# Kernel tuning notes

Hardware: AMD Instinct MI355X
Metric: run time of the kernel (lower is better)

The kernel has to match this reference:

```python
import jax, jax.numpy as jnp
import numpy as np
import math

CHANNELS = 1024
NUM_HEADS = 16
HEAD_DIM = CHANNELS // NUM_HEADS  # 64
ROPE_DIM = int(HEAD_DIM * 0.5)    # 32
BASE_FREQ = 10000.0


def apply_rope(x):
    """x: [b, h, t, d]; rotate first ROPE_DIM features, pass the rest through."""
    t = x.shape[2]
    half = ROPE_DIM // 2
    theta = 1.0 / (BASE_FREQ ** (jnp.arange(0, ROPE_DIM, 2, dtype=jnp.float32) / ROPE_DIM))  # [half]
    ang = jnp.arange(t, dtype=jnp.float32)[:, None] * theta[None, :]  # [t, half]
    ang = jnp.concatenate([ang, ang], axis=-1)  # [t, ROPE_DIM]
    cos = jnp.cos(ang)[None, None, :, :]
    sin = jnp.sin(ang)[None, None, :, :]
    x_rope, x_pass = x[..., :ROPE_DIM], x[..., ROPE_DIM:]
    neg_half = jnp.concatenate([-x_rope[..., half:], x_rope[..., :half]], axis=-1)
    x_rope = x_rope * cos + neg_half * sin
    return jnp.concatenate([x_rope, x_pass], axis=-1)


def proximal_bias(length):
    pos = jnp.arange(length, dtype=jnp.float32)
    diff = pos[None, :] - pos[:, None]
    return -jnp.log1p(jnp.abs(diff))[None, None, :, :]  # [1,1,t,t]


def conv1x1(x, w, b):
    """x: [b, c_in, t], w: [c_out, c_in], b: [c_out] -> [b, c_out, t]"""
    return jnp.einsum('oc,bct->bot', w, x) + b[None, :, None]


def setup_inputs() -> dict:
    key = jax.random.key(0)
    ks = jax.random.split(key, 10)
    B, C, T = 8, CHANNELS, 1024
    scale = 1.0 / math.sqrt(C)
    return {
        "x": jax.random.normal(ks[0], (B, C, T), dtype=jnp.float32),
        "context": jax.random.normal(ks[1], (B, C, T), dtype=jnp.float32),
        "attention_mask": jnp.ones((B, 1, 1, T), dtype=jnp.int32),
        "Wq": jax.random.normal(ks[2], (C, C), dtype=jnp.float32) * scale,
        "bq": jnp.zeros((C,), dtype=jnp.float32),
        "Wk": jax.random.normal(ks[3], (C, C), dtype=jnp.float32) * scale,
        "bk": jnp.zeros((C,), dtype=jnp.float32),
        "Wv": jax.random.normal(ks[4], (C, C), dtype=jnp.float32) * scale,
        "bv": jnp.zeros((C,), dtype=jnp.float32),
        "Wo": jax.random.normal(ks[5], (C, C), dtype=jnp.float32) * scale,
        "bo": jnp.zeros((C,), dtype=jnp.float32),
    }


def reference(x, context, attention_mask, Wq, bq, Wk, bk, Wv, bv, Wo, bo):
    B, C, T = x.shape
    H, D = NUM_HEADS, HEAD_DIM
    q = conv1x1(x, Wq, bq)
    k = conv1x1(context, Wk, bk)
    v = conv1x1(context, Wv, bv)
    # b (h d) t -> b h t d
    def split_heads(z):
        return z.reshape(B, H, D, -1).transpose(0, 1, 3, 2)
    q, k, v = split_heads(q), split_heads(k), split_heads(v)
    q = apply_rope(q)
    k = apply_rope(k)
    scores = jnp.einsum('bhqd,bhkd->bhqk', q, k) / math.sqrt(D)
    scores = scores + proximal_bias(T)  # proximal_bias=True, self-attention
    scores = jnp.where(attention_mask == 0, jnp.float32(-10000.0), scores)
    probs = jax.nn.softmax(scores, axis=-1)  # dropout_rate=0.0 -> identity
    out = jnp.einsum('bhqk,bhkd->bhqd', probs, v)
    # b h q d -> b (h d) q
    out = out.transpose(0, 1, 3, 2).reshape(B, C, T)
    return conv1x1(out, Wo, bo)
```

## Files before the change

kernel.cpp:

```cpp
#include <hip/hip_runtime.h>
#include <hip/hip_bf16.h>
#include <math.h>

#define BB 8
#define CC 1024
#define TT 1024
#define HH 16
#define DD 64

typedef __attribute__((ext_vector_type(8))) short short8;
typedef __attribute__((ext_vector_type(4))) short short4_;
typedef __attribute__((ext_vector_type(4))) float f32x4;
typedef __attribute__((ext_vector_type(4))) int   i32x4;
typedef __attribute__((ext_vector_type(2))) unsigned long long u64x2;

#define QSCALE 0.18033688f

__device__ __forceinline__ unsigned short f2bf(float f) {
    unsigned u = __builtin_bit_cast(unsigned, f);
    u += 0x7fffu + ((u >> 16) & 1u);
    return (unsigned short)(u >> 16);
}

__device__ __forceinline__ f32x4 mfma16(short8 a, short8 b, f32x4 c) {
    return __builtin_amdgcn_mfma_f32_16x16x32_bf16(a, b, c, 0, 0, 0);
}

__device__ __forceinline__ void async16(const void* g, void* l) {
    __builtin_amdgcn_global_load_lds(
        (const __attribute__((address_space(1))) unsigned int*)g,
        (__attribute__((address_space(3))) unsigned int*)l, 16, 0, 0);
}

__device__ __forceinline__ unsigned cvtpk(float lo, float hi) {
    unsigned r;
    asm("v_cvt_pk_bf16_f32 %0, %1, %2" : "=v"(r) : "v"(lo), "v"(hi));
    return r;
}

__global__ __launch_bounds__(256) void cast_w_kernel(
    const float* __restrict__ Wq, const float* __restrict__ Wk,
    const float* __restrict__ Wv, const float* __restrict__ Wo,
    unsigned short* __restrict__ dst)
{
    const int z = blockIdx.y;
    const float* W = (z == 0) ? Wq : (z == 1) ? Wk : (z == 2) ? Wv : Wo;
    unsigned short* d = dst + (size_t)z * CC * CC;
    int idx = blockIdx.x * 256 + threadIdx.x;
    float4 f = ((const float4*)W)[idx];
    short4_ s;
    s[0] = (short)f2bf(f.x); s[1] = (short)f2bf(f.y);
    s[2] = (short)f2bf(f.z); s[3] = (short)f2bf(f.w);
    ((short4_*)d)[idx] = s;
}

__global__ __launch_bounds__(256) void tcast2_kernel(
    const float* __restrict__ x, const float* __restrict__ ctx,
    unsigned short* __restrict__ xT, unsigned short* __restrict__ cTo)
{
    __shared__ float sT[64][65];
    const int tid = threadIdx.x;
    const int z = blockIdx.z;
    const float* in = (z < BB) ? x : ctx;
    unsigned short* out = (z < BB) ? xT : cTo;
    const int b = (z < BB) ? z : z - BB;
    const int tB = blockIdx.x * 64, cT = blockIdx.y * 64;

    const float* ib = in + ((size_t)b * CC + cT) * TT + tB;
    const int r = tid >> 2;
    #pragma unroll
    for (int j = 0; j < 4; j++) {
        int t4 = (tid & 3) * 4 + j * 16;
        float4 f = *(const float4*)(ib + (size_t)r * TT + t4);
        sT[r][t4 + 0] = f.x; sT[r][t4 + 1] = f.y;
        sT[r][t4 + 2] = f.z; sT[r][t4 + 3] = f.w;
    }
    __syncthreads();
    const int t_l = tid >> 2, cch = (tid & 3) * 16;
    short8 o0, o1;
    #pragma unroll
    for (int i = 0; i < 8; i++) {
        o0[i] = (short)f2bf(sT[cch + i][t_l]);
        o1[i] = (short)f2bf(sT[cch + 8 + i][t_l]);
    }
    unsigned short* dp = out + ((size_t)b * TT + tB + t_l) * CC + cT + cch;
    *(short8*)dp = o0;
    *(short8*)(dp + 8) = o1;
}

__global__ __launch_bounds__(256) void tcast_kernel(
    const float* __restrict__ in, unsigned short* __restrict__ out)
{
    __shared__ float sT[64][65];
    const int tid = threadIdx.x;
    const int tB = blockIdx.x * 64, cT = blockIdx.y * 64, b = blockIdx.z;

    const float* ib = in + ((size_t)b * CC + cT) * TT + tB;
    const int r = tid >> 2;
    #pragma unroll
    for (int j = 0; j < 4; j++) {
        int t4 = (tid & 3) * 4 + j * 16;
        float4 f = *(const float4*)(ib + (size_t)r * TT + t4);
        sT[r][t4 + 0] = f.x; sT[r][t4 + 1] = f.y;
        sT[r][t4 + 2] = f.z; sT[r][t4 + 3] = f.w;
    }
    __syncthreads();
    const int t_l = tid >> 2, cch = (tid & 3) * 16;
    short8 o0, o1;
    #pragma unroll
    for (int i = 0; i < 8; i++) {
        o0[i] = (short)f2bf(sT[cch + i][t_l]);
        o1[i] = (short)f2bf(sT[cch + 8 + i][t_l]);
    }
    unsigned short* dp = out + ((size_t)b * TT + tB + t_l) * CC + cT + cch;
    *(short8*)dp = o0;
    *(short8*)(dp + 8) = o1;
}

__global__ __launch_bounds__(256) void qkv_gll_kernel(
    const unsigned short* __restrict__ xT, const unsigned short* __restrict__ cT,
    const unsigned short* __restrict__ Wq2, const unsigned short* __restrict__ Wk2,
    const unsigned short* __restrict__ Wv2,
    const float* __restrict__ bq, const float* __restrict__ bk,
    const float* __restrict__ bv,
    unsigned short* __restrict__ qo, unsigned short* __restrict__ ko,
    unsigned short* __restrict__ vo,
    int mode)
{
    __shared__ __align__(16) short smem[4 * 64 * 72];

    const int tid = threadIdx.x, lane = tid & 63, wave = tid >> 6;
    const int wm = wave >> 1, wn = wave & 1;
    const int l15 = lane & 15, lq = lane >> 4;

    const int zz = blockIdx.x, tTile = blockIdx.y, oTile = blockIdx.z;
    int w, b;
    if (mode == 0)      { w = zz % 3;        b = zz / 3;  }
    else if (mode == 1) { w = 0;             b = zz;      }
    else                { w = 1 + (zz & 1);  b = zz >> 1; }
    const unsigned short* inT = (w == 0) ? xT : cT;
    const int oBase = oTile * 128, tBase = tTile * 128;

    const unsigned short* WA = (w == 0) ? Wq2 : (w == 1) ? Wk2 : Wv2;
    const float* bias        = (w == 0) ? bq  : (w == 1) ? bk  : bv;

    const int srow = lane >> 2;
    const int sch  = (lane ^ (lane >> 2) ^ (lane >> 4)) & 3;
    const unsigned short* gA0 = WA + (size_t)(oBase + wave * 32 + srow) * CC + sch * 8;
    const unsigned short* gA1 = gA0 + (size_t)16 * CC;
    const unsigned short* gB0 = inT + ((size_t)b * TT + tBase + wave * 32 + srow) * CC + sch * 8;
    const unsigned short* gB1 = gB0 + (size_t)16 * CC;

    short* A0b = smem;            short* B0b = smem + 4096;
    short* A1b = smem + 8192;     short* B1b = smem + 12288;
    const int oA0 = (wave * 2 + 0) * 512;
    const int oA1 = (wave * 2 + 1) * 512;

    const int csw = ((lq ^ (l15 & 3) ^ (l15 >> 2)) & 3) * 8;

    f32x4 acc[4][4];
    #pragma unroll
    for (int mt = 0; mt < 4; mt++)
        #pragma unroll
        for (int nt = 0; nt < 4; nt++) acc[mt][nt] = (f32x4){0.f, 0.f, 0.f, 0.f};

    auto stage = [&](int c0, short* dA, short* dB) {
        async16(gA0 + c0, dA + oA0);
        async16(gA1 + c0, dA + oA1);
        async16(gB0 + c0, dB + oA0);
        async16(gB1 + c0, dB + oA1);
    };
    auto compute = [&](const short* bA, const short* bB) {
        short8 af[4], bf[4];
        #pragma unroll
        for (int mt = 0; mt < 4; mt++)
            af[mt] = *(const short8*)(bA + (wm * 64 + mt * 16 + l15) * 32 + csw);
        #pragma unroll
        for (int nt = 0; nt < 4; nt++)
            bf[nt] = *(const short8*)(bB + (wn * 64 + nt * 16 + l15) * 32 + csw);
        #pragma unroll
        for (int mt = 0; mt < 4; mt++)
            #pragma unroll
            for (int nt = 0; nt < 4; nt++)
                acc[mt][nt] = mfma16(af[mt], bf[nt], acc[mt][nt]);
    };

    stage(0, A0b, B0b);

    #pragma unroll 1
    for (int tt = 0; tt < 16; tt++) {
        const int c = tt * 64;
        asm volatile("s_waitcnt vmcnt(0)" ::: "memory");
        __builtin_amdgcn_s_barrier();
        __builtin_amdgcn_sched_barrier(0);
        stage(c + 32, A1b, B1b);
        compute(A0b, B0b);
        asm volatile("s_waitcnt lgkmcnt(0)" ::: "memory");

        asm volatile("s_waitcnt vmcnt(0)" ::: "memory");
        __builtin_amdgcn_s_barrier();
        __builtin_amdgcn_sched_barrier(0);
        if (tt < 15) stage(c + 64, A0b, B0b);
        compute(A1b, B1b);
        asm volatile("s_waitcnt lgkmcnt(0)" ::: "memory");
    }
    __syncthreads();

    #pragma unroll
    for (int mt = 0; mt < 4; mt++)
        #pragma unroll
        for (int r = 0; r < 4; r++) {
            float bi = bias[oBase + wm * 64 + mt * 16 + lq * 4 + r];
            #pragma unroll
            for (int nt = 0; nt < 4; nt++) {
                acc[mt][nt][r] += bi;
                if (w == 0) acc[mt][nt][r] *= QSCALE;
            }
        }

    const int h = oTile * 2 + wm;
    short* sT = smem + wave * (64 * 72);

    if (w < 2) {
        #pragma unroll
        for (int r = 0; r < 4; r++) {
            float dr = (float)(lq * 4 + r);
            float theta = exp2f(dr * -0.8304820237f);
            float sa, ca, ss, cs;
            sincosf((float)(tBase + wn * 64 + l15) * theta, &sa, &ca);
            sincosf(16.0f * theta, &ss, &cs);
            #pragma unroll
            for (int nt = 0; nt < 4; nt++) {
                float x0 = acc[0][nt][r], x1 = acc[1][nt][r];
                acc[0][nt][r] = x0 * ca - x1 * sa;
                acc[1][nt][r] = x1 * ca + x0 * sa;
                float c2 = ca * cs - sa * ss;
                sa = sa * cs + ca * ss;
                ca = c2;
            }
        }
        #pragma unroll
        for (int nt = 0; nt < 4; nt++)
            #pragma unroll
            for (int mt = 0; mt < 4; mt++) {
                short4_ v4;
                #pragma unroll
                for (int r = 0; r < 4; r++) v4[r] = (short)f2bf(acc[mt][nt][r]);
                *(short4_*)(sT + (nt * 16 + l15) * 72 + mt * 16 + lq * 4) = v4;
            }
    } else {
        #pragma unroll
        for (int mt = 0; mt < 4; mt++)
            #pragma unroll
            for (int r = 0; r < 4; r++)
                #pragma unroll
                for (int nt = 0; nt < 4; nt++)
                    sT[(mt * 16 + lq * 4 + r) * 72 + nt * 16 + l15] =
                        (short)f2bf(acc[mt][nt][r]);
    }
    __asm__ volatile("s_waitcnt lgkmcnt(0)" ::: "memory");

    unsigned short* dstBase;
    if (w == 0)
        dstBase = qo + ((size_t)(b * HH + h) * TT + tBase + wn * 64 + lane) * DD;
    else if (w == 1)
        dstBase = ko + ((size_t)(b * HH + h) * TT + tBase + wn * 64 + lane) * DD;
    else
        dstBase = vo + ((size_t)(b * HH + h) * DD + lane) * TT + tBase + wn * 64;
    #pragma unroll
    for (int j = 0; j < 8; j++)
        *(short8*)(dstBase + j * 8) = *(short8*)(sT + lane * 72 + j * 8);
}

__global__ __launch_bounds__(256) void oproj_gll_kernel(
    const unsigned short* __restrict__ att, const unsigned short* __restrict__ Wo2,
    const float* __restrict__ bo, float* __restrict__ out)
{
    __shared__ __align__(16) short smem[16384];

    const int tid = threadIdx.x, lane = tid & 63, wave = tid >> 6;
    const int wm = wave >> 1, wn = wave & 1;
    const int l15 = lane & 15, lq = lane >> 4;
    const int b = blockIdx.x, tTile = blockIdx.y, oTile = blockIdx.z;
    const int oBase = oTile * 128, tBase = tTile * 128;

    const int srow = lane >> 2;
    const int sch  = (lane ^ (lane >> 2) ^ (lane >> 4)) & 3;
    const unsigned short* gA0 = Wo2 + (size_t)(oBase + wave * 32 + srow) * CC + sch * 8;
    const unsigned short* gA1 = gA0 + (size_t)16 * CC;
    const unsigned short* attB = att + (size_t)b * HH * TT * DD;
    const int t0 = tBase + wave * 32 + srow;
    const int csch = sch * 8;

    short* A0b = smem;            short* B0b = smem + 4096;
    short* A1b = smem + 8192;     short* B1b = smem + 12288;
    const int oA0 = (wave * 2 + 0) * 512;
    const int oA1 = (wave * 2 + 1) * 512;

    const int csw = ((lq ^ (l15 & 3) ^ (l15 >> 2)) & 3) * 8;

    f32x4 acc[4][4];
    #pragma unroll
    for (int mt = 0; mt < 4; mt++)
        #pragma unroll
        for (int nt = 0; nt < 4; nt++) acc[mt][nt] = (f32x4){0.f, 0.f, 0.f, 0.f};

    auto stage = [&](int c0, short* dA, short* dB) {
        int c = c0 + csch;
        const unsigned short* g0 =
            attB + ((size_t)(c >> 6) * TT + t0) * DD + (c & 63);
        async16(gA0 + c0, dA + oA0);
        async16(gA1 + c0, dA + oA1);
        async16(g0, dB + oA0);
        async16(g0 + 16 * DD, dB + oA1);
    };
    auto compute = [&](const short* bA, const short* bB) {
        short8 af[4], bf[4];
        #pragma unroll
        for (int mt = 0; mt < 4; mt++)
            af[mt] = *(const short8*)(bA + (wm * 64 + mt * 16 + l15) * 32 + csw);
        #pragma unroll
        for (int nt = 0; nt < 4; nt++)
            bf[nt] = *(const short8*)(bB + (wn * 64 + nt * 16 + l15) * 32 + csw);
        #pragma unroll
        for (int mt = 0; mt < 4; mt++)
            #pragma unroll
            for (int nt = 0; nt < 4; nt++)
                acc[mt][nt] = mfma16(af[mt], bf[nt], acc[mt][nt]);
    };

    stage(0, A0b, B0b);

    #pragma unroll 1
    for (int tt = 0; tt < 16; tt++) {
        const int c = tt * 64;
        asm volatile("s_waitcnt vmcnt(0)" ::: "memory");
        __builtin_amdgcn_s_barrier();
        __builtin_amdgcn_sched_barrier(0);
        stage(c + 32, A1b, B1b);
        compute(A0b, B0b);
        asm volatile("s_waitcnt lgkmcnt(0)" ::: "memory");

        asm volatile("s_waitcnt vmcnt(0)" ::: "memory");
        __builtin_amdgcn_s_barrier();
        __builtin_amdgcn_sched_barrier(0);
        if (tt < 15) stage(c + 64, A0b, B0b);
        compute(A1b, B1b);
        asm volatile("s_waitcnt lgkmcnt(0)" ::: "memory");
    }

    #pragma unroll
    for (int mt = 0; mt < 4; mt++)
        #pragma unroll
        for (int r = 0; r < 4; r++) {
            int o = oBase + wm * 64 + mt * 16 + lq * 4 + r;
            float bi = bo[o];
            float* dst = out + ((size_t)b * CC + o) * TT + tBase + wn * 64;
            #pragma unroll
            for (int nt = 0; nt < 4; nt++)
                dst[nt * 16 + l15] = acc[mt][nt][r] + bi;
        }
}

__global__ __launch_bounds__(256) void attn_mfma_kernel(
    const unsigned short* __restrict__ q, const unsigned short* __restrict__ k,
    const unsigned short* __restrict__ v, const int* __restrict__ mask,
    unsigned short* __restrict__ att)
{
    __shared__ __align__(16) short sQw[64 * 72];
    __shared__ __align__(16) short sK[64 * 72];
    __shared__ __align__(16) short sV[64 * 72];
    __shared__ int sOK[4];

    const int tid = threadIdx.x, lane = tid & 63, wq = tid >> 6;
    const int l15 = lane & 15, lq = lane >> 4;
    const int bh = blockIdx.x, qTile = blockIdx.y, b = bh >> 4;

    const int sr = tid >> 2, sc = (tid & 3) * 16;
    const int* maskB = mask + b * TT;

    {
        i32x4 m4 = *(const i32x4*)(maskB + tid * 4);
        int ok = (m4[0] != 0) & (m4[1] != 0) & (m4[2] != 0) & (m4[3] != 0);
        unsigned long long bal = __ballot(ok);
        if (lane == 0) sOK[wq] = (bal == ~0ull);
    }

    {
        const unsigned short* gq = q + ((size_t)bh * TT + qTile * 64 + sr) * DD + sc;
        *(short8*)(sQw + sr * 72 + sc)     = *(const short8*)gq;
        *(short8*)(sQw + sr * 72 + sc + 8) = *(const short8*)(gq + 8);
    }
    __syncthreads();

    const short8 bq0 = *(short8*)(sQw + (wq * 16 + l15) * 72 + lq * 8);
    const short8 bq1 = *(short8*)(sQw + (wq * 16 + l15) * 72 + 32 + lq * 8);
    const bool allOK = sOK[0] && sOK[1] && sOK[2] && sOK[3];
    __syncthreads();

    float* wtab = (float*)sQw;
    #pragma unroll
    for (int j = 0; j < 8; j++) {
        int d = tid + 256 * j;
        int ad = d - 1023; ad = ad < 0 ? -ad : ad;
        wtab[d] = __builtin_amdgcn_rcpf(1.0f + (float)ad);
    }

    short8 vones;
    #pragma unroll
    for (int e = 0; e < 8; e++) vones[e] = (short)0x3F80;

    f32x4 accO[4];
    #pragma unroll
    for (int nt = 0; nt < 4; nt++) accO[nt] = (f32x4){0.f, 0.f, 0.f, 0.f};
    f32x4 accD = (f32x4){0.f, 0.f, 0.f, 0.f};

    const int qpos = qTile * 64 + wq * 16 + l15;
    const unsigned short* kB = k + (size_t)bh * TT * DD;
    const unsigned short* vB = v + (size_t)bh * DD * TT;

    const int xo = ((tid & 3) >> 1) * 8 + (tid & 1) * 4;
    short* vwp = sV + sr * 72 + xo;

    const unsigned short* gk = kB + (size_t)sr * DD + sc;
    const unsigned short* gv = vB + (size_t)sr * TT + sc;
    short8 kr0 = *(const short8*)gk;
    short8 kr1 = *(const short8*)(gk + 8);
    short8 vr0 = *(const short8*)gv;
    short8 vr1 = *(const short8*)(gv + 8);

    for (int kt = 0; kt < 16; kt++) {
        __syncthreads();
        *(short8*)(sK + sr * 72 + sc)     = kr0;
        *(short8*)(sK + sr * 72 + sc + 8) = kr1;
        {
            u64x2 vv0 = __builtin_bit_cast(u64x2, vr0);
            u64x2 vv1 = __builtin_bit_cast(u64x2, vr1);
            *(unsigned long long*)(vwp)      = vv0[0];
            *(unsigned long long*)(vwp + 16) = vv0[1];
            *(unsigned long long*)(vwp + 32) = vv1[0];
            *(unsigned long long*)(vwp + 48) = vv1[1];
        }
        __syncthreads();

        if (kt < 15) {
            gk += 64 * DD;
            gv += 64;
            kr0 = *(const short8*)gk;
            kr1 = *(const short8*)(gk + 8);
            vr0 = *(const short8*)gv;
            vr1 = *(const short8*)(gv + 8);
        }

        f32x4 s4[4];
        #pragma unroll
        for (int nt = 0; nt < 4; nt++) {
            short8 ka0 = *(short8*)(sK + (nt * 16 + l15) * 72 + lq * 8);
            short8 ka1 = *(short8*)(sK + (nt * 16 + l15) * 72 + 32 + lq * 8);
            f32x4 z = (f32x4){0.f, 0.f, 0.f, 0.f};
            z = mfma16(ka0, bq0, z);
            z = mfma16(ka1, bq1, z);
            s4[nt] = z;
        }

        const float* wrow = wtab + (kt * 64 + lq * 4 + 1023 - qpos);
        unsigned pk8[4][2];
        if (allOK) {
            #pragma unroll
            for (int nt = 0; nt < 4; nt++) {
                #pragma unroll
                for (int h2 = 0; h2 < 2; h2++) {
                    float p0 = __builtin_amdgcn_exp2f(s4[nt][2 * h2])
                               * wrow[nt * 16 + 2 * h2];
                    float p1 = __builtin_amdgcn_exp2f(s4[nt][2 * h2 + 1])
                               * wrow[nt * 16 + 2 * h2 + 1];
                    pk8[nt][h2] = cvtpk(p0, p1);
                }
            }
        } else {
            #pragma unroll
            for (int nt = 0; nt < 4; nt++) {
                i32x4 mk = *(const i32x4*)(maskB + kt * 64 + nt * 16 + lq * 4);
                #pragma unroll
                for (int h2 = 0; h2 < 2; h2++) {
                    float p0 = __builtin_amdgcn_exp2f(s4[nt][2 * h2])
                               * wrow[nt * 16 + 2 * h2];
                    float p1 = __builtin_amdgcn_exp2f(s4[nt][2 * h2 + 1])
                               * wrow[nt * 16 + 2 * h2 + 1];
                    p0 = mk[2 * h2]     ? p0 : 0.f;
                    p1 = mk[2 * h2 + 1] ? p1 : 0.f;
                    pk8[nt][h2] = cvtpk(p0, p1);
                }
            }
        }

        i32x4 c0 = {(int)pk8[0][0], (int)pk8[0][1], (int)pk8[1][0], (int)pk8[1][1]};
        i32x4 c1 = {(int)pk8[2][0], (int)pk8[2][1], (int)pk8[3][0], (int)pk8[3][1]};
        short8 ap0 = __builtin_bit_cast(short8, c0);
        short8 ap1 = __builtin_bit_cast(short8, c1);

        accD = mfma16(ap0, vones, accD);
        accD = mfma16(ap1, vones, accD);

        #pragma unroll
        for (int nt = 0; nt < 4; nt++) {
            const short* vrow = sV + (nt * 16 + l15) * 72 + lq * 16;
            short8 b0 = *(short8*)(vrow);
            short8 b1 = *(short8*)(vrow + 8);
            accO[nt] = mfma16(ap0, b0, accO[nt]);
            accO[nt] = mfma16(ap1, b1, accO[nt]);
        }
    }

    unsigned short* aB = att + ((size_t)bh * TT + qTile * 64 + wq * 16 + lq * 4) * DD;
    #pragma unroll
    for (int r = 0; r < 4; r++) {
        float inv = 1.0f / accD[r];
        #pragma unroll
        for (int nt = 0; nt < 4; nt++)
            aB[(size_t)r * DD + nt * 16 + l15] = f2bf(accO[nt][r] * inv);
    }
}

__global__ __launch_bounds__(256) void qkv_mfma_kernel(
    const float* __restrict__ x, const float* __restrict__ ctx,
    const float* __restrict__ Wq, const float* __restrict__ bq,
    const float* __restrict__ Wk, const float* __restrict__ bk,
    const float* __restrict__ Wv, const float* __restrict__ bv,
    unsigned short* __restrict__ qo, unsigned short* __restrict__ ko,
    unsigned short* __restrict__ vo)
{
    __shared__ __align__(16) short smem[4 * 64 * 72];
    short* sA = smem;
    short* sB = smem + 128 * 40;

    const int tid  = threadIdx.x;
    const int lane = tid & 63;
    const int wave = tid >> 6;
    const int wm = wave >> 1, wn = wave & 1;
    const int l15 = lane & 15, lq = lane >> 4;

    const int tTile = blockIdx.x, oTile = blockIdx.y;
    const int b = blockIdx.z / 3, w = blockIdx.z % 3;
    const int oBase = oTile * 128, tBase = tTile * 128;

    const float* In   = (w == 0) ? x  : ctx;
    const float* W    = (w == 0) ? Wq : (w == 1) ? Wk : Wv;
    const float* bias = (w == 0) ? bq : (w == 1) ? bk : bv;
    const float* InB  = In + (size_t)b * CC * TT;

    const int ao = tid >> 1, ak = (tid & 1) * 16;
    const int bt = tid & 127, bk_ = (tid >> 7) * 16;
    const float* gA = W + (size_t)(oBase + ao) * CC + ak;
    const float* gB = InB + (size_t)bk_ * TT + tBase + bt;

    f32x4 acc[4][4];
    #pragma unroll
    for (int mt = 0; mt < 4; mt++)
        #pragma unroll
        for (int nt = 0; nt < 4; nt++) acc[mt][nt] = (f32x4){0.f, 0.f, 0.f, 0.f};

    for (int c0 = 0; c0 < CC; c0 += 32) {
        float fa[16], fb[16];
        #pragma unroll
        for (int i = 0; i < 4; i++) {
            float4 t4 = *(const float4*)(gA + c0 + 4 * i);
            fa[4*i+0] = t4.x; fa[4*i+1] = t4.y; fa[4*i+2] = t4.z; fa[4*i+3] = t4.w;
        }
        #pragma unroll
        for (int j = 0; j < 16; j++)
            fb[j] = gB[(size_t)(c0 + j) * TT];

        __syncthreads();
        short8 pa0, pa1, pb0, pb1;
        #pragma unroll
        for (int e = 0; e < 8; e++) {
            pa0[e] = (short)f2bf(fa[e]);   pa1[e] = (short)f2bf(fa[8 + e]);
            pb0[e] = (short)f2bf(fb[e]);   pb1[e] = (short)f2bf(fb[8 + e]);
        }
        *(short8*)(sA + ao * 40 + ak)     = pa0;
        *(short8*)(sA + ao * 40 + ak + 8) = pa1;
        *(short8*)(sB + bt * 40 + bk_)     = pb0;
        *(short8*)(sB + bt * 40 + bk_ + 8) = pb1;
        __syncthreads();

        short8 af[4], bf[4];
        #pragma unroll
        for (int mt = 0; mt < 4; mt++)
            af[mt] = *(short8*)(sA + (wm * 64 + mt * 16 + l15) * 40 + lq * 8);
        #pragma unroll
        for (int nt = 0; nt < 4; nt++)
            bf[nt] = *(short8*)(sB + (wn * 64 + nt * 16 + l15) * 40 + lq * 8);
        #pragma unroll
        for (int mt = 0; mt < 4; mt++)
            #pragma unroll
            for (int nt = 0; nt < 4; nt++)
                acc[mt][nt] = mfma16(af[mt], bf[nt], acc[mt][nt]);
    }

    #pragma unroll
    for (int mt = 0; mt < 4; mt++)
        #pragma unroll
        for (int r = 0; r < 4; r++) {
            float bi = bias[oBase + wm * 64 + mt * 16 + lq * 4 + r];
            #pragma unroll
            for (int nt = 0; nt < 4; nt++) {
                acc[mt][nt][r] += bi;
                if (w == 0) acc[mt][nt][r] *= QSCALE;
            }
        }

    const int h = oTile * 2 + wm;
    __syncthreads();
    short* sT = smem + wave * (64 * 72);

    if (w < 2) {
        #pragma unroll
        for (int r = 0; r < 4; r++) {
            float theta = powf(10000.0f, -(float)(lq * 4 + r) * (1.0f / 16.0f));
            #pragma unroll
            for (int nt = 0; nt < 4; nt++) {
                float tpos = (float)(tBase + wn * 64 + nt * 16 + l15);
                float sa, ca;
                sincosf(tpos * theta, &sa, &ca);
                float x0 = acc[0][nt][r], x1 = acc[1][nt][r];
                acc[0][nt][r] = x0 * ca - x1 * sa;
                acc[1][nt][r] = x1 * ca + x0 * sa;
            }
        }
        #pragma unroll
        for (int nt = 0; nt < 4; nt++)
            #pragma unroll
            for (int mt = 0; mt < 4; mt++) {
                short4_ v4;
                #pragma unroll
                for (int r = 0; r < 4; r++) v4[r] = (short)f2bf(acc[mt][nt][r]);
                *(short4_*)(sT + (nt * 16 + l15) * 72 + mt * 16 + lq * 4) = v4;
            }
    } else {
        #pragma unroll
        for (int mt = 0; mt < 4; mt++)
            #pragma unroll
            for (int r = 0; r < 4; r++)
                #pragma unroll
                for (int nt = 0; nt < 4; nt++)
                    sT[(mt * 16 + lq * 4 + r) * 72 + nt * 16 + l15] =
                        (short)f2bf(acc[mt][nt][r]);
    }
    __asm__ volatile("s_waitcnt lgkmcnt(0)" ::: "memory");

    unsigned short* dstBase;
    if (w == 0)
        dstBase = qo + ((size_t)(b * HH + h) * TT + tBase + wn * 64 + lane) * DD;
    else if (w == 1)
        dstBase = ko + ((size_t)(b * HH + h) * TT + tBase + wn * 64 + lane) * DD;
    else
        dstBase = vo + ((size_t)(b * HH + h) * DD + lane) * TT + tBase + wn * 64;
    #pragma unroll
    for (int j = 0; j < 8; j++)
        *(short8*)(dstBase + j * 8) = *(short8*)(sT + lane * 72 + j * 8);
}

__global__ __launch_bounds__(256) void oproj_mfma_kernel(
    const unsigned short* __restrict__ att, const float* __restrict__ Wo,
    const float* __restrict__ bo, float* __restrict__ out)
{
    __shared__ __align__(16) short smem[2 * 128 * 40];
    short* sA = smem;
    short* sB = smem + 128 * 40;

    const int tid = threadIdx.x, lane = tid & 63, wave = tid >> 6;
    const int wm = wave >> 1, wn = wave & 1;
    const int l15 = lane & 15, lq = lane >> 4;
    const int tTile = blockIdx.x, oTile = blockIdx.y, b = blockIdx.z;
    const int oBase = oTile * 128, tBase = tTile * 128;

    const int ao = tid >> 1, ak = (tid & 1) * 16;
    const int bt = tid & 127, bk_ = (tid >> 7) * 16;
    const float* gA = Wo + (size_t)(oBase + ao) * CC + ak;

    f32x4 acc[4][4];
    #pragma unroll
    for (int mt = 0; mt < 4; mt++)
        #pragma unroll
        for (int nt = 0; nt < 4; nt++) acc[mt][nt] = (f32x4){0.f, 0.f, 0.f, 0.f};

    for (int c0 = 0; c0 < CC; c0 += 32) {
        float fa[16];
        #pragma unroll
        for (int i = 0; i < 4; i++) {
            float4 t4 = *(const float4*)(gA + c0 + 4 * i);
            fa[4*i+0] = t4.x; fa[4*i+1] = t4.y; fa[4*i+2] = t4.z; fa[4*i+3] = t4.w;
        }
        int c = c0 + bk_;
        const unsigned short* gB =
            att + (((size_t)b * HH + (c >> 6)) * TT + tBase + bt) * DD + (c & 63);
        short8 pb0 = *(const short8*)gB;
        short8 pb1 = *(const short8*)(gB + 8);

        __syncthreads();
        short8 pa0, pa1;
        #pragma unroll
        for (int e = 0; e < 8; e++) {
            pa0[e] = (short)f2bf(fa[e]); pa1[e] = (short)f2bf(fa[8 + e]);
        }
        *(short8*)(sA + ao * 40 + ak)      = pa0;
        *(short8*)(sA + ao * 40 + ak + 8)  = pa1;
        *(short8*)(sB + bt * 40 + bk_)     = pb0;
        *(short8*)(sB + bt * 40 + bk_ + 8) = pb1;
        __syncthreads();

        short8 af[4], bf[4];
        #pragma unroll
        for (int mt = 0; mt < 4; mt++)
            af[mt] = *(short8*)(sA + (wm * 64 + mt * 16 + l15) * 40 + lq * 8);
        #pragma unroll
        for (int nt = 0; nt < 4; nt++)
            bf[nt] = *(short8*)(sB + (wn * 64 + nt * 16 + l15) * 40 + lq * 8);
        #pragma unroll
        for (int mt = 0; mt < 4; mt++)
            #pragma unroll
            for (int nt = 0; nt < 4; nt++)
                acc[mt][nt] = mfma16(af[mt], bf[nt], acc[mt][nt]);
    }

    #pragma unroll
    for (int mt = 0; mt < 4; mt++)
        #pragma unroll
        for (int r = 0; r < 4; r++) {
            int o = oBase + wm * 64 + mt * 16 + lq * 4 + r;
            float bi = bo[o];
            float* dst = out + ((size_t)b * CC + o) * TT + tBase + wn * 64;
            #pragma unroll
            for (int nt = 0; nt < 4; nt++)
                dst[nt * 16 + l15] = acc[mt][nt][r] + bi;
        }
}

extern "C" void kernel_launch(void* const* d_in, const int* in_sizes, int n_in,
                              void* d_out, int out_size, void* d_ws, size_t ws_size,
                              hipStream_t stream)
{
    const float* x   = (const float*)d_in[0];
    const float* ctx = (const float*)d_in[1];
    const int* mask  = (const int*)d_in[2];
    const float* Wq  = (const float*)d_in[3];
    const float* bq  = (const float*)d_in[4];
    const float* Wk  = (const float*)d_in[5];
    const float* bk  = (const float*)d_in[6];
    const float* Wv  = (const float*)d_in[7];
    const float* bv  = (const float*)d_in[8];
    const float* Wo  = (const float*)d_in[9];
    const float* bo  = (const float*)d_in[10];
    float* out = (float*)d_out;

    const size_t nq = (size_t)BB * HH * TT * DD;
    const size_t nw = (size_t)CC * CC;

    if (ws_size >= (5 * nq + 4 * nw) * sizeof(unsigned short)) {
        unsigned short* q   = (unsigned short*)d_ws;
        unsigned short* k   = q + nq;
        unsigned short* v   = k + nq;
        unsigned short* xT  = v + nq;
        unsigned short* cT  = xT + nq;
        unsigned short* Wb  = cT + nq;
        unsigned short* Wqb = Wb;
        unsigned short* Wkb = Wb + nw;
        unsigned short* Wvb = Wb + 2 * nw;
        unsigned short* Wob = Wb + 3 * nw;

        cast_w_kernel<<<dim3(1024, 4), 256, 0, stream>>>(Wq, Wk, Wv, Wo, Wb);
        tcast2_kernel<<<dim3(16, 16, BB * 2), 256, 0, stream>>>(x, ctx, xT, cT);
        qkv_gll_kernel<<<dim3(BB * 3, 8, 8), 256, 0, stream>>>(
            xT, cT, Wqb, Wkb, Wvb, bq, bk, bv, q, k, v, 0);
        attn_mfma_kernel<<<dim3(BB * HH, TT / 64), 256, 0, stream>>>(
            q, k, v, mask, xT);
        oproj_gll_kernel<<<dim3(BB, 8, 8), 256, 0, stream>>>(xT, Wob, bo, out);
    } else if (ws_size >= (4 * nq + 4 * nw) * sizeof(unsigned short)) {
        unsigned short* q   = (unsigned short*)d_ws;
        unsigned short* k   = q + nq;
        unsigned short* v   = k + nq;
        unsigned short* buf = v + nq;
        unsigned short* Wb  = buf + nq;
        unsigned short* Wqb = Wb;
        unsigned short* Wkb = Wb + nw;
        unsigned short* Wvb = Wb + 2 * nw;
        unsigned short* Wob = Wb + 3 * nw;

        cast_w_kernel<<<dim3(1024, 4), 256, 0, stream>>>(Wq, Wk, Wv, Wo, Wb);
        tcast_kernel<<<dim3(16, 16, BB), 256, 0, stream>>>(x, buf);
        qkv_gll_kernel<<<dim3(BB, 8, 8), 256, 0, stream>>>(
            buf, buf, Wqb, Wkb, Wvb, bq, bk, bv, q, k, v, 1);
        tcast_kernel<<<dim3(16, 16, BB), 256, 0, stream>>>(ctx, buf);
        qkv_gll_kernel<<<dim3(BB * 2, 8, 8), 256, 0, stream>>>(
            buf, buf, Wqb, Wkb, Wvb, bq, bk, bv, q, k, v, 2);
        attn_mfma_kernel<<<dim3(BB * HH, TT / 64), 256, 0, stream>>>(
            q, k, v, mask, buf);
        oproj_gll_kernel<<<dim3(BB, 8, 8), 256, 0, stream>>>(buf, Wob, bo, out);
    } else {
        unsigned short* q   = (unsigned short*)d_ws;
        unsigned short* k   = q + nq;
        unsigned short* v   = k + nq;
        unsigned short* att = v + nq;
        qkv_mfma_kernel<<<dim3(8, 8, BB * 3), 256, 0, stream>>>(
            x, ctx, Wq, bq, Wk, bk, Wv, bv, q, k, v);
        attn_mfma_kernel<<<dim3(BB * HH, TT / 64), 256, 0, stream>>>(
            q, k, v, mask, att);
        oproj_mfma_kernel<<<dim3(8, 8, BB), 256, 0, stream>>>(att, Wo, bo, out);
    }
}
```

Measured before the change: 303.3 us.

## Triple-buffer QKV GEMM loads with vmcnt-based waits and reorder grid dims

Replaces the double-buffered K-loop in the QKV projection with a three-stage ring of LDS buffers. Each step prefetches two tiles ahead and waits with partial vmcnt counts instead of draining all loads, so global-memory latency can overlap more MFMA work. The launch grid is also reordered so tile indices run fastest and batch/weight select is on z, which changes block scheduling order and L2 reuse. LDS use rises (3*8192 shorts) and the epilogue staging buffer now reuses a differently sized smem array, which could hurt occupancy or correctness if the epilogue needs more space.

```diff
diff --git a/kernel.cpp b/kernel.cpp
--- a/kernel.cpp
+++ b/kernel.cpp
@@ -127,13 +127,14 @@
     unsigned short* __restrict__ vo,
     int mode)
 {
-    __shared__ __align__(16) short smem[4 * 64 * 72];
+    __shared__ __align__(16) short smem[3 * 8192];
 
     const int tid = threadIdx.x, lane = tid & 63, wave = tid >> 6;
     const int wm = wave >> 1, wn = wave & 1;
     const int l15 = lane & 15, lq = lane >> 4;
 
-    const int zz = blockIdx.x, tTile = blockIdx.y, oTile = blockIdx.z;
+    const int tTile = blockIdx.x, oTile = blockIdx.y;
+    const int zz = blockIdx.z;
     int w, b;
     if (mode == 0)      { w = zz % 3;        b = zz / 3;  }
     else if (mode == 1) { w = 0;             b = zz;      }
@@ -151,8 +152,9 @@
     const unsigned short* gB0 = inT + ((size_t)b * TT + tBase + wave * 32 + srow) * CC + sch * 8;
     const unsigned short* gB1 = gB0 + (size_t)16 * CC;
 
-    short* A0b = smem;            short* B0b = smem + 4096;
-    short* A1b = smem + 8192;     short* B1b = smem + 12288;
+    short* cA = smem;             short* cB = smem + 4096;
+    short* nA = smem + 8192;      short* nB = smem + 12288;
+    short* pA = smem + 16384;     short* pB = smem + 20480;
     const int oA0 = (wave * 2 + 0) * 512;
     const int oA1 = (wave * 2 + 1) * 512;
 
@@ -164,47 +166,46 @@
         #pragma unroll
         for (int nt = 0; nt < 4; nt++) acc[mt][nt] = (f32x4){0.f, 0.f, 0.f, 0.f};
 
-    auto stage = [&](int c0, short* dA, short* dB) {
-        async16(gA0 + c0, dA + oA0);
-        async16(gA1 + c0, dA + oA1);
-        async16(gB0 + c0, dB + oA0);
-        async16(gB1 + c0, dB + oA1);
-    };
-    auto compute = [&](const short* bA, const short* bB) {
+    async16(gA0, cA + oA0);       async16(gA1, cA + oA1);
+    async16(gB0, cB + oA0);       async16(gB1, cB + oA1);
+    async16(gA0 + 32, nA + oA0);  async16(gA1 + 32, nA + oA1);
+    async16(gB0 + 32, nB + oA0);  async16(gB1 + 32, nB + oA1);
+
+    for (int t = 0; t < 32; t++) {
+        if (t < 30) {
+            int c2 = (t + 2) * 32;
+            async16(gA0 + c2, pA + oA0);
+            async16(gA1 + c2, pA + oA1);
+            async16(gB0 + c2, pB + oA0);
+            async16(gB1 + c2, pB + oA1);
+        }
+        __builtin_amdgcn_sched_barrier(0);
+        if (t < 30)       asm volatile("s_waitcnt vmcnt(8)" ::: "memory");
+        else if (t == 30) asm volatile("s_waitcnt vmcnt(4)" ::: "memory");
+        else              asm volatile("s_waitcnt vmcnt(0)" ::: "memory");
+        __builtin_amdgcn_s_barrier();
+        __builtin_amdgcn_sched_barrier(0);
+
         short8 af[4], bf[4];
         #pragma unroll
         for (int mt = 0; mt < 4; mt++)
-            af[mt] = *(const short8*)(bA + (wm * 64 + mt * 16 + l15) * 32 + csw);
+            af[mt] = *(short8*)(cA + (wm * 64 + mt * 16 + l15) * 32 + csw);
         #pragma unroll
         for (int nt = 0; nt < 4; nt++)
-            bf[nt] = *(const short8*)(bB + (wn * 64 + nt * 16 + l15) * 32 + csw);
+            bf[nt] = *(short8*)(cB + (wn * 64 + nt * 16 + l15) * 32 + csw);
         #pragma unroll
         for (int mt = 0; mt < 4; mt++)
             #pragma unroll
             for (int nt = 0; nt < 4; nt++)
                 acc[mt][nt] = mfma16(af[mt], bf[nt], acc[mt][nt]);
-    };
-
-    stage(0, A0b, B0b);
-
-    #pragma unroll 1
-    for (int tt = 0; tt < 16; tt++) {
-        const int c = tt * 64;
-        asm volatile("s_waitcnt vmcnt(0)" ::: "memory");
+
+        __builtin_amdgcn_sched_barrier(0);
+        asm volatile("s_waitcnt lgkmcnt(0)" ::: "memory");
         __builtin_amdgcn_s_barrier();
-        __builtin_amdgcn_sched_barrier(0);
-        stage(c + 32, A1b, B1b);
-        compute(A0b, B0b);
-        asm volatile("s_waitcnt lgkmcnt(0)" ::: "memory");
-
-        asm volatile("s_waitcnt vmcnt(0)" ::: "memory");
-        __builtin_amdgcn_s_barrier();
-        __builtin_amdgcn_sched_barrier(0);
-        if (tt < 15) stage(c + 64, A0b, B0b);
-        compute(A1b, B1b);
-        asm volatile("s_waitcnt lgkmcnt(0)" ::: "memory");
-    }
-    __syncthreads();
+
+        short* tA = cA; cA = nA; nA = pA; pA = tA;
+        short* tB = cB; cB = nB; nB = pB; pB = tB;
+    }
 
     #pragma unroll
     for (int mt = 0; mt < 4; mt++)
@@ -771,7 +772,7 @@
 
         cast_w_kernel<<<dim3(1024, 4), 256, 0, stream>>>(Wq, Wk, Wv, Wo, Wb);
         tcast2_kernel<<<dim3(16, 16, BB * 2), 256, 0, stream>>>(x, ctx, xT, cT);
-        qkv_gll_kernel<<<dim3(BB * 3, 8, 8), 256, 0, stream>>>(
+        qkv_gll_kernel<<<dim3(8, 8, BB * 3), 256, 0, stream>>>(
             xT, cT, Wqb, Wkb, Wvb, bq, bk, bv, q, k, v, 0);
         attn_mfma_kernel<<<dim3(BB * HH, TT / 64), 256, 0, stream>>>(
             q, k, v, mask, xT);
@@ -789,10 +790,10 @@
 
         cast_w_kernel<<<dim3(1024, 4), 256, 0, stream>>>(Wq, Wk, Wv, Wo, Wb);
         tcast_kernel<<<dim3(16, 16, BB), 256, 0, stream>>>(x, buf);
-        qkv_gll_kernel<<<dim3(BB, 8, 8), 256, 0, stream>>>(
+        qkv_gll_kernel<<<dim3(8, 8, BB), 256, 0, stream>>>(
             buf, buf, Wqb, Wkb, Wvb, bq, bk, bv, q, k, v, 1);
         tcast_kernel<<<dim3(16, 16, BB), 256, 0, stream>>>(ctx, buf);
-        qkv_gll_kernel<<<dim3(BB * 2, 8, 8), 256, 0, stream>>>(
+        qkv_gll_kernel<<<dim3(8, 8, BB * 2), 256, 0, stream>>>(
             buf, buf, Wqb, Wkb, Wvb, bq, bk, bv, q, k, v, 2);
         attn_mfma_kernel<<<dim3(BB * HH, TT / 64), 256, 0, stream>>>(
             q, k, v, mask, buf);
```

New measurement: 295.2 us. -2.7%, faster.

## Enlarge projection GEMM tiles to 256x128 with 512-thread blocks

Applied to the files above, without the earlier changes.

The QKV and output projection kernels move from 256-thread blocks with 128x128 output tiles to 512-thread blocks with 256x128 tiles. The input (B-side) tile is shared by 8 waves instead of 4, so each activation row is loaded half as often. The grid is reordered so tiles along t vary fastest, which may change L2 reuse of the weights. The QKV epilogue now writes through shared memory in two passes because the transpose scratch only fits 4 waves at a time, adding barriers. Larger blocks also mean fewer blocks in the grid and more LDS per block, which can lower occupancy.

```diff
diff --git a/kernel.cpp b/kernel.cpp
--- a/kernel.cpp
+++ b/kernel.cpp
@@ -117,7 +117,7 @@
     *(short8*)(dp + 8) = o1;
 }
 
-__global__ __launch_bounds__(256) void qkv_gll_kernel(
+__global__ __launch_bounds__(512) void qkv_gll_kernel(
     const unsigned short* __restrict__ xT, const unsigned short* __restrict__ cT,
     const unsigned short* __restrict__ Wq2, const unsigned short* __restrict__ Wk2,
     const unsigned short* __restrict__ Wv2,
@@ -127,19 +127,20 @@
     unsigned short* __restrict__ vo,
     int mode)
 {
-    __shared__ __align__(16) short smem[4 * 64 * 72];
+    __shared__ __align__(16) short smem[24576];
 
     const int tid = threadIdx.x, lane = tid & 63, wave = tid >> 6;
     const int wm = wave >> 1, wn = wave & 1;
     const int l15 = lane & 15, lq = lane >> 4;
 
-    const int zz = blockIdx.x, tTile = blockIdx.y, oTile = blockIdx.z;
+    const int tTile = blockIdx.x, oTile = blockIdx.y;
+    const int zz = blockIdx.z;
     int w, b;
     if (mode == 0)      { w = zz % 3;        b = zz / 3;  }
     else if (mode == 1) { w = 0;             b = zz;      }
     else                { w = 1 + (zz & 1);  b = zz >> 1; }
     const unsigned short* inT = (w == 0) ? xT : cT;
-    const int oBase = oTile * 128, tBase = tTile * 128;
+    const int oBase = oTile * 256, tBase = tTile * 128;
 
     const unsigned short* WA = (w == 0) ? Wq2 : (w == 1) ? Wk2 : Wv2;
     const float* bias        = (w == 0) ? bq  : (w == 1) ? bk  : bv;
@@ -148,13 +149,10 @@
     const int sch  = (lane ^ (lane >> 2) ^ (lane >> 4)) & 3;
     const unsigned short* gA0 = WA + (size_t)(oBase + wave * 32 + srow) * CC + sch * 8;
     const unsigned short* gA1 = gA0 + (size_t)16 * CC;
-    const unsigned short* gB0 = inT + ((size_t)b * TT + tBase + wave * 32 + srow) * CC + sch * 8;
-    const unsigned short* gB1 = gB0 + (size_t)16 * CC;
-
-    short* A0b = smem;            short* B0b = smem + 4096;
-    short* A1b = smem + 8192;     short* B1b = smem + 12288;
-    const int oA0 = (wave * 2 + 0) * 512;
-    const int oA1 = (wave * 2 + 1) * 512;
+    const unsigned short* gB0 = inT + ((size_t)b * TT + tBase + wave * 16 + srow) * CC + sch * 8;
+
+    short* b0A = smem;            short* b0B = smem + 8192;
+    short* b1A = smem + 12288;    short* b1B = smem + 20480;
 
     const int csw = ((lq ^ (l15 & 3) ^ (l15 >> 2)) & 3) * 8;
 
@@ -165,10 +163,9 @@
         for (int nt = 0; nt < 4; nt++) acc[mt][nt] = (f32x4){0.f, 0.f, 0.f, 0.f};
 
     auto stage = [&](int c0, short* dA, short* dB) {
-        async16(gA0 + c0, dA + oA0);
-        async16(gA1 + c0, dA + oA1);
-        async16(gB0 + c0, dB + oA0);
-        async16(gB1 + c0, dB + oA1);
+        async16(gA0 + c0, dA + (wave * 2 + 0) * 512);
+        async16(gA1 + c0, dA + (wave * 2 + 1) * 512);
+        async16(gB0 + c0, dB + wave * 512);
     };
     auto compute = [&](const short* bA, const short* bB) {
         short8 af[4], bf[4];
@@ -185,7 +182,7 @@
                 acc[mt][nt] = mfma16(af[mt], bf[nt], acc[mt][nt]);
     };
 
-    stage(0, A0b, B0b);
+    stage(0, b0A, b0B);
 
     #pragma unroll 1
     for (int tt = 0; tt < 16; tt++) {
@@ -193,15 +190,15 @@
         asm volatile("s_waitcnt vmcnt(0)" ::: "memory");
         __builtin_amdgcn_s_barrier();
         __builtin_amdgcn_sched_barrier(0);
-        stage(c + 32, A1b, B1b);
-        compute(A0b, B0b);
+        stage(c + 32, b1A, b1B);
+        compute(b0A, b0B);
         asm volatile("s_waitcnt lgkmcnt(0)" ::: "memory");
 
         asm volatile("s_waitcnt vmcnt(0)" ::: "memory");
         __builtin_amdgcn_s_barrier();
         __builtin_amdgcn_sched_barrier(0);
-        if (tt < 15) stage(c + 64, A0b, B0b);
-        compute(A1b, B1b);
+        if (tt < 15) stage(c + 64, b0A, b0B);
+        compute(b1A, b1B);
         asm volatile("s_waitcnt lgkmcnt(0)" ::: "memory");
     }
     __syncthreads();
@@ -218,8 +215,8 @@
             }
         }
 
-    const int h = oTile * 2 + wm;
-    short* sT = smem + wave * (64 * 72);
+    const int h = oTile * 4 + wm;
+    short* sT = smem + (wave & 3) * 4608;
 
     if (w < 2) {
         #pragma unroll
@@ -239,26 +236,7 @@
                 ca = c2;
             }
         }
-        #pragma unroll
-        for (int nt = 0; nt < 4; nt++)
-            #pragma unroll
-            for (int mt = 0; mt < 4; mt++) {
-                short4_ v4;
-                #pragma unroll
-                for (int r = 0; r < 4; r++) v4[r] = (short)f2bf(acc[mt][nt][r]);
-                *(short4_*)(sT + (nt * 16 + l15) * 72 + mt * 16 + lq * 4) = v4;
-            }
-    } else {
-        #pragma unroll
-        for (int mt = 0; mt < 4; mt++)
-            #pragma unroll
-            for (int r = 0; r < 4; r++)
-                #pragma unroll
-                for (int nt = 0; nt < 4; nt++)
-                    sT[(mt * 16 + lq * 4 + r) * 72 + nt * 16 + l15] =
-                        (short)f2bf(acc[mt][nt][r]);
-    }
-    __asm__ volatile("s_waitcnt lgkmcnt(0)" ::: "memory");
+    }
 
     unsigned short* dstBase;
     if (w == 0)
@@ -267,35 +245,60 @@
         dstBase = ko + ((size_t)(b * HH + h) * TT + tBase + wn * 64 + lane) * DD;
     else
         dstBase = vo + ((size_t)(b * HH + h) * DD + lane) * TT + tBase + wn * 64;
-    #pragma unroll
-    for (int j = 0; j < 8; j++)
-        *(short8*)(dstBase + j * 8) = *(short8*)(sT + lane * 72 + j * 8);
-}
-
-__global__ __launch_bounds__(256) void oproj_gll_kernel(
+
+    #pragma unroll 1
+    for (int pass = 0; pass < 2; pass++) {
+        if ((wave >> 2) == pass) {
+            if (w < 2) {
+                #pragma unroll
+                for (int nt = 0; nt < 4; nt++)
+                    #pragma unroll
+                    for (int mt = 0; mt < 4; mt++) {
+                        short4_ v4;
+                        #pragma unroll
+                        for (int r = 0; r < 4; r++) v4[r] = (short)f2bf(acc[mt][nt][r]);
+                        *(short4_*)(sT + (nt * 16 + l15) * 72 + mt * 16 + lq * 4) = v4;
+                    }
+            } else {
+                #pragma unroll
+                for (int mt = 0; mt < 4; mt++)
+                    #pragma unroll
+                    for (int r = 0; r < 4; r++)
+                        #pragma unroll
+                        for (int nt = 0; nt < 4; nt++)
+                            sT[(mt * 16 + lq * 4 + r) * 72 + nt * 16 + l15] =
+                                (short)f2bf(acc[mt][nt][r]);
+            }
+            __asm__ volatile("s_waitcnt lgkmcnt(0)" ::: "memory");
+            #pragma unroll
+            for (int j = 0; j < 8; j++)
+                *(short8*)(dstBase + j * 8) = *(short8*)(sT + lane * 72 + j * 8);
+        }
+        __syncthreads();
+    }
+}
+
+__global__ __launch_bounds__(512) void oproj_gll_kernel(
     const unsigned short* __restrict__ att, const unsigned short* __restrict__ Wo2,
     const float* __restrict__ bo, float* __restrict__ out)
 {
-    __shared__ __align__(16) short smem[16384];
+    __shared__ __align__(16) short smem[24576];
 
     const int tid = threadIdx.x, lane = tid & 63, wave = tid >> 6;
     const int wm = wave >> 1, wn = wave & 1;
     const int l15 = lane & 15, lq = lane >> 4;
     const int b = blockIdx.x, tTile = blockIdx.y, oTile = blockIdx.z;
-    const int oBase = oTile * 128, tBase = tTile * 128;
+    const int oBase = oTile * 256, tBase = tTile * 128;
 
     const int srow = lane >> 2;
     const int sch  = (lane ^ (lane >> 2) ^ (lane >> 4)) & 3;
     const unsigned short* gA0 = Wo2 + (size_t)(oBase + wave * 32 + srow) * CC + sch * 8;
     const unsigned short* gA1 = gA0 + (size_t)16 * CC;
     const unsigned short* attB = att + (size_t)b * HH * TT * DD;
-    const int t0 = tBase + wave * 32 + srow;
-    const int csch = sch * 8;
-
-    short* A0b = smem;            short* B0b = smem + 4096;
-    short* A1b = smem + 8192;     short* B1b = smem + 12288;
-    const int oA0 = (wave * 2 + 0) * 512;
-    const int oA1 = (wave * 2 + 1) * 512;
+    const unsigned short* gB0 = attB + (size_t)(tBase + wave * 16 + srow) * DD + sch * 8;
+
+    short* b0A = smem;            short* b0B = smem + 8192;
+    short* b1A = smem + 12288;    short* b1B = smem + 20480;
 
     const int csw = ((lq ^ (l15 & 3) ^ (l15 >> 2)) & 3) * 8;
 
@@ -306,13 +309,11 @@
         for (int nt = 0; nt < 4; nt++) acc[mt][nt] = (f32x4){0.f, 0.f, 0.f, 0.f};
 
     auto stage = [&](int c0, short* dA, short* dB) {
-        int c = c0 + csch;
-        const unsigned short* g0 =
-            attB + ((size_t)(c >> 6) * TT + t0) * DD + (c & 63);
-        async16(gA0 + c0, dA + oA0);
-        async16(gA1 + c0, dA + oA1);
-        async16(g0, dB + oA0);
-        async16(g0 + 16 * DD, dB + oA1);
+        async16(gA0 + c0, dA + (wave * 2 + 0) * 512);
+        async16(gA1 + c0, dA + (wave * 2 + 1) * 512);
+        const unsigned short* gb =
+            gB0 + (size_t)(c0 >> 6) * TT * DD + (c0 & 63);
+        async16(gb, dB + wave * 512);
     };
     auto compute = [&](const short* bA, const short* bB) {
         short8 af[4], bf[4];
@@ -329,7 +330,7 @@
                 acc[mt][nt] = mfma16(af[mt], bf[nt], acc[mt][nt]);
     };
 
-    stage(0, A0b, B0b);
+    stage(0, b0A, b0B);
 
     #pragma unroll 1
     for (int tt = 0; tt < 16; tt++) {
@@ -337,15 +338,15 @@
         asm volatile("s_waitcnt vmcnt(0)" ::: "memory");
         __builtin_amdgcn_s_barrier();
         __builtin_amdgcn_sched_barrier(0);
-        stage(c + 32, A1b, B1b);
-        compute(A0b, B0b);
+        stage(c + 32, b1A, b1B);
+        compute(b0A, b0B);
         asm volatile("s_waitcnt lgkmcnt(0)" ::: "memory");
 
         asm volatile("s_waitcnt vmcnt(0)" ::: "memory");
         __builtin_amdgcn_s_barrier();
         __builtin_amdgcn_sched_barrier(0);
-        if (tt < 15) stage(c + 64, A0b, B0b);
-        compute(A1b, B1b);
+        if (tt < 15) stage(c + 64, b0A, b0B);
+        compute(b1A, b1B);
         asm volatile("s_waitcnt lgkmcnt(0)" ::: "memory");
     }
 
@@ -771,11 +772,11 @@
 
         cast_w_kernel<<<dim3(1024, 4), 256, 0, stream>>>(Wq, Wk, Wv, Wo, Wb);
         tcast2_kernel<<<dim3(16, 16, BB * 2), 256, 0, stream>>>(x, ctx, xT, cT);
-        qkv_gll_kernel<<<dim3(BB * 3, 8, 8), 256, 0, stream>>>(
+        qkv_gll_kernel<<<dim3(8, 4, BB * 3), 512, 0, stream>>>(
             xT, cT, Wqb, Wkb, Wvb, bq, bk, bv, q, k, v, 0);
         attn_mfma_kernel<<<dim3(BB * HH, TT / 64), 256, 0, stream>>>(
             q, k, v, mask, xT);
-        oproj_gll_kernel<<<dim3(BB, 8, 8), 256, 0, stream>>>(xT, Wob, bo, out);
+        oproj_gll_kernel<<<dim3(BB, 8, 4), 512, 0, stream>>>(xT, Wob, bo, out);
     } else if (ws_size >= (4 * nq + 4 * nw) * sizeof(unsigned short)) {
         unsigned short* q   = (unsigned short*)d_ws;
         unsigned short* k   = q + nq;
@@ -789,14 +790,14 @@
 
         cast_w_kernel<<<dim3(1024, 4), 256, 0, stream>>>(Wq, Wk, Wv, Wo, Wb);
         tcast_kernel<<<dim3(16, 16, BB), 256, 0, stream>>>(x, buf);
-        qkv_gll_kernel<<<dim3(BB, 8, 8), 256, 0, stream>>>(
+        qkv_gll_kernel<<<dim3(8, 4, BB), 512, 0, stream>>>(
             buf, buf, Wqb, Wkb, Wvb, bq, bk, bv, q, k, v, 1);
         tcast_kernel<<<dim3(16, 16, BB), 256, 0, stream>>>(ctx, buf);
-        qkv_gll_kernel<<<dim3(BB * 2, 8, 8), 256, 0, stream>>>(
+        qkv_gll_kernel<<<dim3(8, 4, BB * 2), 512, 0, stream>>>(
             buf, buf, Wqb, Wkb, Wvb, bq, bk, bv, q, k, v, 2);
         attn_mfma_kernel<<<dim3(BB * HH, TT / 64), 256, 0, stream>>>(
             q, k, v, mask, buf);
-        oproj_gll_kernel<<<dim3(BB, 8, 8), 256, 0, stream>>>(buf, Wob, bo, out);
+        oproj_gll_kernel<<<dim3(BB, 8, 4), 512, 0, stream>>>(buf, Wob, bo, out);
     } else {
         unsigned short* q   = (unsigned short*)d_ws;
         unsigned short* k   = q + nq;
```

New measurement: 302.0 us. No clear change (-0.4%).
